# Optimization experiments

Hardware: AMD Instinct MI355X
Metric: run time of the kernel (lower is better)

Reference implementation:

```python
import jax, jax.numpy as jnp
import numpy as np

B, V, T, N, F, M = 1, 100000, 2, 32, 64, 1600000


def setup_inputs() -> dict:
    key = jax.random.key(0)
    k_adj, k_v0, k_n0, k_f0, k_v1, k_n1, k_f1 = jax.random.split(key, 7)
    adjacency = jax.random.randint(k_adj, (B, V, T, N), -8, N, dtype=jnp.int32)

    def make_indices(kv, kn):
        b = jnp.zeros((M,), dtype=jnp.int32)  # B == 1
        v = jax.random.randint(kv, (M,), 0, V, dtype=jnp.int32)
        n = jax.random.randint(kn, (M,), 0, N, dtype=jnp.int32)
        return jnp.stack([b, v, n], axis=-1)  # [M, 3]

    indices0 = make_indices(k_v0, k_n0)
    indices1 = make_indices(k_v1, k_n1)
    features0 = jax.random.normal(k_f0, (M, F), dtype=jnp.float32)
    features1 = jax.random.normal(k_f1, (M, F), dtype=jnp.float32)
    return {"adjacency": adjacency, "indices0": indices0, "features0": features0,
            "indices1": indices1, "features1": features1}


def reference(adjacency, indices0, features0, indices1, features1):
    # adjacency: [B, V, T, N]; indices_i: [M, 3] (b, v, n); features_i: [M, F]
    use_sum = False
    Bv, Vv = adjacency.shape[0], adjacency.shape[1]
    # degree[b, v, t] = number of valid (>= 0) neighbor slots, clamped to >= 1
    degree = jnp.maximum(jnp.sum(adjacency >= 0, axis=-1), 1).astype(features0.dtype)  # [B, V, T]

    def aggr(indices, features, t):
        # scatter_nd into [B, V, N, F] then sum over N == segment-sum over (b, v)
        seg = indices[:, 0] * Vv + indices[:, 1]  # flattened (b, v)
        summed = jax.ops.segment_sum(features, seg, num_segments=Bv * Vv)
        summed = summed.reshape(Bv, Vv, features.shape[-1])  # [B, V, F]
        if use_sum:
            return summed
        return summed / degree[:, :, t][..., None]

    out0 = aggr(indices0, features0, 0)
    out1 = aggr(indices1, features1, 1)
    return (out0, out1)
```

## Files before the change

kernel.cpp:

```cpp
#include <hip/hip_runtime.h>

#define V_CONST 100000
#define T_CONST 2
#define N_CONST 32
#define F_CONST 64
#define PAD 64

__global__ void degree_kernel(const int* __restrict__ adj,
                              float* __restrict__ rdeg, int VT) {
    int i = blockIdx.x * blockDim.x + threadIdx.x;
    if (i >= VT) return;
    const int4* a = (const int4*)(adj + (size_t)i * N_CONST);
    int cnt = 0;
#pragma unroll
    for (int j = 0; j < N_CONST / 4; ++j) {
        int4 x = a[j];
        cnt += (x.x >= 0) + (x.y >= 0) + (x.z >= 0) + (x.w >= 0);
    }
    if (cnt < 1) cnt = 1;
    int v = i / T_CONST;
    int t = i - v * T_CONST;
    rdeg[t * V_CONST + v] = 1.0f / (float)cnt;
}

__global__ void fill_kernel(const int* __restrict__ idx,
                            int* __restrict__ counts,
                            int* __restrict__ ids, int M) {
    int m = blockIdx.x * blockDim.x + threadIdx.x;
    if (m >= M) return;
    int v = idx[m * 3 + 1];
    int pos = atomicAdd(&counts[v], 1);
    if (pos < PAD) ids[(size_t)v * PAD + pos] = m;
}

__global__ void gather_kernel(const float* __restrict__ feat,
                              const int* __restrict__ ids,
                              const int* __restrict__ counts,
                              const float* __restrict__ rdeg,
                              float* __restrict__ out, int V) {
    int gid = blockIdx.x * blockDim.x + threadIdx.x;
    int v = gid >> 6;
    int lane = gid & 63;
    if (v >= V) return;
    int c = counts[v];
    c = min(c, PAD);
    int myid = ids[(size_t)v * PAD + lane];
    float a0 = 0.f, a1 = 0.f, a2 = 0.f, a3 = 0.f;
    int i = 0;
    for (; i + 4 <= c; i += 4) {
        int r0 = __shfl(myid, i);
        int r1 = __shfl(myid, i + 1);
        int r2 = __shfl(myid, i + 2);
        int r3 = __shfl(myid, i + 3);
        a0 += feat[(size_t)r0 * F_CONST + lane];
        a1 += feat[(size_t)r1 * F_CONST + lane];
        a2 += feat[(size_t)r2 * F_CONST + lane];
        a3 += feat[(size_t)r3 * F_CONST + lane];
    }
    for (; i < c; ++i) {
        int r = __shfl(myid, i);
        a0 += feat[(size_t)r * F_CONST + lane];
    }
    out[(size_t)v * F_CONST + lane] = (a0 + a1 + a2 + a3) * rdeg[v];
}

extern "C" void kernel_launch(void* const* d_in, const int* in_sizes, int n_in,
                              void* d_out, int out_size, void* d_ws, size_t ws_size,
                              hipStream_t stream) {
    const int* adj   = (const int*)d_in[0];
    const int* idx0  = (const int*)d_in[1];
    const float* f0  = (const float*)d_in[2];
    const int* idx1  = (const int*)d_in[3];
    const float* f1  = (const float*)d_in[4];
    float* out = (float*)d_out;

    const int M = in_sizes[1] / 3;
    const int VT = V_CONST * T_CONST;

    char* ws = (char*)d_ws;
    int*   counts = (int*)ws;
    float* rdeg   = (float*)(ws + (size_t)2 * V_CONST * 4);
    int*   ids    = (int*)(ws + (size_t)4 * V_CONST * 4);

    hipMemsetAsync(counts, 0, (size_t)2 * V_CONST * sizeof(int), stream);

    {
        int block = 256;
        int grid = (VT + block - 1) / block;
        degree_kernel<<<grid, block, 0, stream>>>(adj, rdeg, VT);
    }

    {
        int block = 256;
        int grid = (M + block - 1) / block;
        fill_kernel<<<grid, block, 0, stream>>>(idx0, counts, ids, M);
        fill_kernel<<<grid, block, 0, stream>>>(idx1, counts + V_CONST,
                                                ids + (size_t)V_CONST * PAD, M);
    }

    {
        int block = 256;
        int grid = (V_CONST * 64 + block - 1) / block;
        gather_kernel<<<grid, block, 0, stream>>>(f0, ids, counts, rdeg, out, V_CONST);
        gather_kernel<<<grid, block, 0, stream>>>(f1, ids + (size_t)V_CONST * PAD,
                                                  counts + V_CONST, rdeg + V_CONST,
                                                  out + (size_t)V_CONST * F_CONST, V_CONST);
    }
}
```

Before: 1.052 ms.

## Fuse degree into gather, merge fill launches, vectorize feature gathers with float4

Removes the separate degree kernel by computing each vertex's degree inside the gather kernel with a wavefront ballot over the adjacency row. The two fill launches are merged into one, and each thread now reads four index triples with int4 loads. The two gather launches are merged, and each wavefront splits into four 16-lane groups that load float4 rows and combine them with xor shuffles. This cuts launch count and the rdeg round trip and widens memory accesses, at the cost of extra shuffle reductions and only a quarter of lanes writing output. The fill kernel assumes M is divisible by 4.

```diff
diff --git a/kernel.cpp b/kernel.cpp
--- a/kernel.cpp
+++ b/kernel.cpp
@@ -6,62 +6,97 @@
 #define F_CONST 64
 #define PAD 64
 
-__global__ void degree_kernel(const int* __restrict__ adj,
-                              float* __restrict__ rdeg, int VT) {
-    int i = blockIdx.x * blockDim.x + threadIdx.x;
-    if (i >= VT) return;
-    const int4* a = (const int4*)(adj + (size_t)i * N_CONST);
-    int cnt = 0;
-#pragma unroll
-    for (int j = 0; j < N_CONST / 4; ++j) {
-        int4 x = a[j];
-        cnt += (x.x >= 0) + (x.y >= 0) + (x.z >= 0) + (x.w >= 0);
+__global__ void fill4_kernel(const int* __restrict__ idx0,
+                             const int* __restrict__ idx1,
+                             int* __restrict__ counts,
+                             int* __restrict__ ids, int M) {
+    int q = blockIdx.x * blockDim.x + threadIdx.x;
+    int nq = M >> 2;
+    if (q >= 2 * nq) return;
+    int t = q >= nq;
+    int qq = q - t * nq;
+    const int4* __restrict__ idx4 = (const int4*)(t ? idx1 : idx0);
+    int4 A = idx4[(size_t)qq * 3 + 0];
+    int4 Bv = idx4[(size_t)qq * 3 + 1];
+    int4 Cv = idx4[(size_t)qq * 3 + 2];
+    int vs0 = A.y, vs1 = Bv.x, vs2 = Bv.w, vs3 = Cv.z;
+    int* cnt = counts + t * V_CONST;
+    int* idt = ids + (size_t)t * V_CONST * PAD;
+    int base = qq * 4;
+    {
+        int pos = atomicAdd(&cnt[vs0], 1);
+        if (pos < PAD) idt[(size_t)vs0 * PAD + pos] = base + 0;
     }
-    if (cnt < 1) cnt = 1;
-    int v = i / T_CONST;
-    int t = i - v * T_CONST;
-    rdeg[t * V_CONST + v] = 1.0f / (float)cnt;
+    {
+        int pos = atomicAdd(&cnt[vs1], 1);
+        if (pos < PAD) idt[(size_t)vs1 * PAD + pos] = base + 1;
+    }
+    {
+        int pos = atomicAdd(&cnt[vs2], 1);
+        if (pos < PAD) idt[(size_t)vs2 * PAD + pos] = base + 2;
+    }
+    {
+        int pos = atomicAdd(&cnt[vs3], 1);
+        if (pos < PAD) idt[(size_t)vs3 * PAD + pos] = base + 3;
+    }
 }
 
-__global__ void fill_kernel(const int* __restrict__ idx,
-                            int* __restrict__ counts,
-                            int* __restrict__ ids, int M) {
-    int m = blockIdx.x * blockDim.x + threadIdx.x;
-    if (m >= M) return;
-    int v = idx[m * 3 + 1];
-    int pos = atomicAdd(&counts[v], 1);
-    if (pos < PAD) ids[(size_t)v * PAD + pos] = m;
-}
-
-__global__ void gather_kernel(const float* __restrict__ feat,
+__global__ void gather_kernel(const float4* __restrict__ f0,
+                              const float4* __restrict__ f1,
+                              const int* __restrict__ adj,
                               const int* __restrict__ ids,
                               const int* __restrict__ counts,
-                              const float* __restrict__ rdeg,
-                              float* __restrict__ out, int V) {
+                              float4* __restrict__ out) {
     int gid = blockIdx.x * blockDim.x + threadIdx.x;
-    int v = gid >> 6;
+    int w = gid >> 6;
+    if (w >= 2 * V_CONST) return;
     int lane = gid & 63;
-    if (v >= V) return;
-    int c = counts[v];
+    int t = (w >= V_CONST);
+    int v = w - t * V_CONST;
+    const float4* __restrict__ feat = t ? f1 : f0;
+
+    int a = adj[((size_t)v * T_CONST + t) * N_CONST + (lane & 31)];
+    unsigned long long bal = __ballot(a >= 0);
+    int deg = __popcll(bal & 0xffffffffull);
+    if (deg < 1) deg = 1;
+    float rdeg = 1.0f / (float)deg;
+
+    int c = counts[w];
     c = min(c, PAD);
-    int myid = ids[(size_t)v * PAD + lane];
-    float a0 = 0.f, a1 = 0.f, a2 = 0.f, a3 = 0.f;
-    int i = 0;
-    for (; i + 4 <= c; i += 4) {
-        int r0 = __shfl(myid, i);
-        int r1 = __shfl(myid, i + 1);
-        int r2 = __shfl(myid, i + 2);
-        int r3 = __shfl(myid, i + 3);
-        a0 += feat[(size_t)r0 * F_CONST + lane];
-        a1 += feat[(size_t)r1 * F_CONST + lane];
-        a2 += feat[(size_t)r2 * F_CONST + lane];
-        a3 += feat[(size_t)r3 * F_CONST + lane];
+    int myid = ids[(size_t)w * PAD + lane];
+    int sub = lane >> 4;
+    int fl = lane & 15;
+    float4 acc = make_float4(0.f, 0.f, 0.f, 0.f);
+    for (int i = 0; i < c; i += 8) {
+        int j0 = i + sub;
+        int j1 = j0 + 4;
+        int r0 = __shfl(myid, j0);
+        int r1 = __shfl(myid, j1);
+        if (j0 < c) {
+            float4 x = feat[(size_t)r0 * (F_CONST / 4) + fl];
+            acc.x += x.x; acc.y += x.y; acc.z += x.z; acc.w += x.w;
+        }
+        if (j1 < c) {
+            float4 x = feat[(size_t)r1 * (F_CONST / 4) + fl];
+            acc.x += x.x; acc.y += x.y; acc.z += x.z; acc.w += x.w;
+        }
     }
-    for (; i < c; ++i) {
-        int r = __shfl(myid, i);
-        a0 += feat[(size_t)r * F_CONST + lane];
+    acc.x += __shfl_xor(acc.x, 16);
+    acc.y += __shfl_xor(acc.y, 16);
+    acc.z += __shfl_xor(acc.z, 16);
+    acc.w += __shfl_xor(acc.w, 16);
+    acc.x += __shfl_xor(acc.x, 32);
+    acc.y += __shfl_xor(acc.y, 32);
+    acc.z += __shfl_xor(acc.z, 32);
+    acc.w += __shfl_xor(acc.w, 32);
+    if (sub == 0) {
+        float4 o;
+        o.x = acc.x * rdeg;
+        o.y = acc.y * rdeg;
+        o.z = acc.z * rdeg;
+        o.w = acc.w * rdeg;
+        out[(size_t)w * (F_CONST / 4) + fl] = o;
     }
-    out[(size_t)v * F_CONST + lane] = (a0 + a1 + a2 + a3) * rdeg[v];
 }
 
 extern "C" void kernel_launch(void* const* d_in, const int* in_sizes, int n_in,
@@ -75,35 +110,26 @@
     float* out = (float*)d_out;
 
     const int M = in_sizes[1] / 3;
-    const int VT = V_CONST * T_CONST;
 
     char* ws = (char*)d_ws;
-    int*   counts = (int*)ws;
-    float* rdeg   = (float*)(ws + (size_t)2 * V_CONST * 4);
-    int*   ids    = (int*)(ws + (size_t)4 * V_CONST * 4);
+    int* counts = (int*)ws;
+    int* ids    = (int*)(ws + (size_t)2 * V_CONST * 4);
 
     hipMemsetAsync(counts, 0, (size_t)2 * V_CONST * sizeof(int), stream);
 
     {
         int block = 256;
-        int grid = (VT + block - 1) / block;
-        degree_kernel<<<grid, block, 0, stream>>>(adj, rdeg, VT);
+        int total = 2 * (M >> 2);
+        int grid = (total + block - 1) / block;
+        fill4_kernel<<<grid, block, 0, stream>>>(idx0, idx1, counts, ids, M);
     }
 
     {
         int block = 256;
-        int grid = (M + block - 1) / block;
-        fill_kernel<<<grid, block, 0, stream>>>(idx0, counts, ids, M);
-        fill_kernel<<<grid, block, 0, stream>>>(idx1, counts + V_CONST,
-                                                ids + (size_t)V_CONST * PAD, M);
-    }
-
-    {
-        int block = 256;
-        int grid = (V_CONST * 64 + block - 1) / block;
-        gather_kernel<<<grid, block, 0, stream>>>(f0, ids, counts, rdeg, out, V_CONST);
-        gather_kernel<<<grid, block, 0, stream>>>(f1, ids + (size_t)V_CONST * PAD,
-                                                  counts + V_CONST, rdeg + V_CONST,
-                                                  out + (size_t)V_CONST * F_CONST, V_CONST);
+        long long threads = (long long)2 * V_CONST * 64;
+        int grid = (int)((threads + block - 1) / block);
+        gather_kernel<<<grid, block, 0, stream>>>((const float4*)f0, (const float4*)f1,
+                                                  adj, ids, counts,
+                                                  (float4*)out);
     }
 }
```

Measured after the change: 1.076 ms. 2.3% more time.
